# Optimization experiments

Measured on AMD Instinct MI355X. Metric: run time of the kernel, lower is better.

The kernel has to match this reference:

```python
import jax, jax.numpy as jnp
import numpy as np

K = 32            # spatial kernel: neighbors per anchor
STRIDE = 4        # spatial_stride -> S = N // 4 anchors
TK_HALF = 1       # temporal_kernel_size=3 -> window offsets -1,0,+1


def setup_inputs() -> dict:
    key = jax.random.key(0)
    k1, k2, k3 = jax.random.split(key, 3)
    points = jax.random.normal(k1, (2, 4, 8192, 6), dtype=jnp.float32)
    # conv_d: Conv2d(4 -> 64, 1x1, bias=False) as a dense matrix [out,in]
    Wd = jax.random.normal(k2, (64, 4), dtype=jnp.float32) * 0.1
    # mlp: Conv2d(64 -> 128, 1x1, bias=False)
    Wm = jax.random.normal(k3, (128, 64), dtype=jnp.float32) * 0.1
    return {"points": points, "Wd": Wd, "Wm": Wm}


def _fps(xyz, npoint):
    """Farthest point sampling on a single frame. xyz: [N,3] -> idx [npoint] int32.
    Deterministic start at index 0."""
    d0 = jnp.sum((xyz - xyz[0]) ** 2, axis=-1)  # [N]

    def body(dists, _):
        nxt = jnp.argmax(dists)
        d = jnp.sum((xyz - xyz[nxt]) ** 2, axis=-1)
        return jnp.minimum(dists, d), nxt.astype(jnp.int32)

    _, idxs = jax.lax.scan(body, d0, None, length=npoint - 1)
    return jnp.concatenate([jnp.zeros((1,), jnp.int32), idxs])


def _knn_idx(neighbor_xyz, anchor_xyz, k):
    """Adaptive ball query realized as k-nearest-neighbors.
    neighbor_xyz: [B,N,3], anchor_xyz: [B,S,3] -> idx [B,S,k]."""
    d2 = jnp.sum((anchor_xyz[:, :, None, :] - neighbor_xyz[:, None, :, :]) ** 2, axis=-1)  # [B,S,N]
    _, idx = jax.lax.top_k(-d2, k)
    return idx


def _group(pts, idx):
    """pts: [B,N,C], idx: [B,S,K] -> [B,S,K,C] gather per batch."""
    return jax.vmap(lambda p, i: p[i])(pts, idx)


def reference(points, Wd, Wm):
    xyzs = points[..., :3]                       # [B,L,N,3] (rgb unused when in_planes==0)
    B, L, N, _ = xyzs.shape
    S = N // STRIDE
    # replicate temporal padding [1,1]
    pad = jnp.concatenate([xyzs[:, :1], xyzs, xyzs[:, -1:]], axis=1)  # [B,L+2,N,3]

    new_xyzs, new_feats = [], []
    for t in range(TK_HALF, L + 2 - TK_HALF):    # anchor frames in padded indexing
        frame = pad[:, t]                        # [B,N,3]
        aidx = jax.vmap(lambda x: _fps(x, S))(frame)       # [B,S]
        anchor = _group(frame, aidx[:, :, None])[:, :, 0]  # [B,S,3]

        fsum = jnp.zeros((B, S, Wm.shape[0]), dtype=points.dtype)
        for di in range(-TK_HALF, TK_HALF + 1):
            nb = pad[:, t + di]                              # [B,N,3]
            idx = _knn_idx(nb, anchor, K)                    # [B,S,K]
            grouped = _group(nb, idx)                        # [B,S,K,3]
            disp = grouped - anchor[:, :, None, :]           # xyz displacement
            tdisp = jnp.full((B, S, K, 1), float(di), dtype=points.dtype)
            d4 = jnp.concatenate([disp, tdisp], axis=-1)     # [B,S,K,4]
            h = jax.nn.relu(jnp.einsum('bskc,oc->bsko', d4, Wd))   # conv_d + ReLU
            h = jax.nn.relu(jnp.einsum('bsko,po->bskp', h, Wm))    # mlp + ReLU
            fsum = fsum + jnp.max(h, axis=2)                 # spatial max-pool, temporal sum
        new_xyzs.append(anchor)
        new_feats.append(fsum)

    new_xyzs = jnp.stack(new_xyzs, axis=1)                   # [B,T,S,3]
    new_feats = jnp.stack(new_feats, axis=1).transpose(0, 1, 3, 2)  # [B,T,C,S]
    return new_xyzs, new_feats
```

## Files before the change

kernel.cpp:

```cpp
#include <hip/hip_runtime.h>
#include <stdint.h>

#define NPTS 8192
#define NS   2048
#define KNNK 32

typedef unsigned long long u64;

__global__ __launch_bounds__(512)
void fps_kernel(const float* __restrict__ pts,
                float* __restrict__ out_xyz)
{
    const int bt  = blockIdx.x;
    const int tid = threadIdx.x;
    const float* frame = pts + (size_t)bt * NPTS * 6;

    __shared__ float4 p4[NPTS];
    __shared__ u64 ring[3];

    float px[16], py[16], pz[16], d[16];
#pragma unroll
    for (int j = 0; j < 16; ++j) {
        int n = j * 512 + tid;
        float x = frame[n*6+0], y = frame[n*6+1], z = frame[n*6+2];
        px[j] = x; py[j] = y; pz[j] = z;
        d[j]  = 3.4028234663852886e38f;
        p4[n] = make_float4(x, y, z, 0.0f);
    }
    if (tid < 3) ring[tid] = 0;
    if (tid == 0) {
        float* ow = out_xyz + (size_t)bt * NS * 3;
        ow[0] = px[0]; ow[1] = py[0]; ow[2] = pz[0];
    }
    __syncthreads();
    float sx = p4[0].x, sy = p4[0].y, sz = p4[0].z;

    int r = 1;
    for (int i = 1; i < NS; ++i) {
        float mloc = 0.0f;
#pragma unroll
        for (int j = 0; j < 16; ++j) {
            float dx = __fsub_rn(px[j], sx);
            float dy = __fsub_rn(py[j], sy);
            float dz = __fsub_rn(pz[j], sz);
            float d2 = __fadd_rn(__fadd_rn(__fmul_rn(dx,dx), __fmul_rn(dy,dy)),
                                 __fmul_rn(dz,dz));
            float nd = fminf(d[j], d2);
            d[j] = nd;
            mloc = fmaxf(mloc, nd);
        }
        int bestn = 0;
#pragma unroll
        for (int j = 15; j >= 0; --j)
            bestn = (d[j] == mloc) ? (j * 512 + tid) : bestn;
        u64 key = ((u64)__float_as_uint(mloc) << 32) | (unsigned)(8191 - bestn);
#pragma unroll
        for (int off = 32; off > 0; off >>= 1) {
            u64 o = __shfl_xor(key, off, 64);
            key = (o > key) ? o : key;
        }
        if ((tid & 63) == 0) atomicMax(&ring[r], key);
        int rn = r + 1; if (rn == 3) rn = 0;
        if (tid == 0) ring[rn] = 0;
        __syncthreads();
        u64 k = ring[r];
        int idx = 8191 - (int)(k & 0xFFFFFFFFu);
        float4 c = p4[idx];
        sx = c.x; sy = c.y; sz = c.z;
        if (tid == 0) {
            float* ow = out_xyz + ((size_t)bt * NS + i) * 3;
            ow[0] = sx; ow[1] = sy; ow[2] = sz;
        }
        r = rn;
    }
}

__device__ __forceinline__ void knn_compact(u64* st, int lane, int& cnt, u64& rk)
{
    for (int e = 0; e < 32; ++e)
        if (e >= cnt) st[(e + 32) * 64 + lane] = ~0ull;
    for (int k = 2; k <= 32; k <<= 1)
        for (int j = k >> 1; j > 0; j >>= 1)
            for (int i = 0; i < 32; ++i) {
                int l = i ^ j;
                if (l > i) {
                    u64 a = st[(i + 32) * 64 + lane];
                    u64 b = st[(l + 32) * 64 + lane];
                    bool asc = ((i & k) == 0);
                    if ((a > b) == asc) {
                        st[(i + 32) * 64 + lane] = b;
                        st[(l + 32) * 64 + lane] = a;
                    }
                }
            }
    for (int i = 0; i < 32; ++i) {
        u64 a = st[i * 64 + lane];
        u64 b = st[(63 - i) * 64 + lane];
        if (b < a) st[i * 64 + lane] = b;
    }
    for (int j = 16; j > 0; j >>= 1)
        for (int i = 0; i < 32; ++i) {
            int l = i ^ j;
            if (l > i) {
                u64 a = st[i * 64 + lane];
                u64 b = st[l * 64 + lane];
                if (a > b) {
                    st[i * 64 + lane] = b;
                    st[l * 64 + lane] = a;
                }
            }
        }
    rk = st[31 * 64 + lane];
    cnt = 0;
}

__global__ __launch_bounds__(64)
void knn_kernel(const float* __restrict__ pts,
                const float* __restrict__ anchors,
                unsigned short* __restrict__ knn_out)
{
    const int blk  = blockIdx.x;
    const int bt   = blk / 96;
    const int r    = blk % 96;
    const int di   = r / 32;
    const int sblk = r % 32;
    const int b = bt >> 2, t0 = bt & 3;
    int lnb = t0 + di - 1; lnb = lnb < 0 ? 0 : (lnb > 3 ? 3 : lnb);
    const float* nb = pts + (size_t)(b * 4 + lnb) * NPTS * 6;
    const int lane = threadIdx.x;
    const int s    = sblk * 64 + lane;

    const float* ap = anchors + ((size_t)bt * NS + s) * 3;
    float ax = ap[0], ay = ap[1], az = ap[2];

    __shared__ u64 st[65 * 64];
    __shared__ float4 tile[512];

    for (int e = 0; e < 64; ++e) st[e * 64 + lane] = ~0ull;
    u64 rk = ~0ull;
    int cnt = 0;

    for (int tb = 0; tb < NPTS; tb += 512) {
        __syncthreads();
#pragma unroll
        for (int q = 0; q < 8; ++q) {
            int c = q * 64 + lane;
            int n = tb + c;
            tile[c] = make_float4(nb[n*6+0], nb[n*6+1], nb[n*6+2], 0.0f);
        }
        __syncthreads();
        for (int c0 = 0; c0 < 512; c0 += 8) {
#pragma unroll
            for (int j = 0; j < 8; ++j) {
                float4 qv = tile[c0 + j];
                float dx = __fsub_rn(ax, qv.x);
                float dy = __fsub_rn(ay, qv.y);
                float dz = __fsub_rn(az, qv.z);
                float d2 = __fadd_rn(__fadd_rn(__fmul_rn(dx,dx), __fmul_rn(dy,dy)),
                                     __fmul_rn(dz,dz));
                u64 key = ((u64)__float_as_uint(d2) << 32)
                        | (unsigned)(tb + c0 + j);
                bool p = key < rk;
                int row = p ? (32 + cnt) : 64;
                st[row * 64 + lane] = key;
                cnt += p ? 1 : 0;
            }
            if (__any(cnt >= 24)) knn_compact(st, lane, cnt, rk);
        }
    }
    knn_compact(st, lane, cnt, rk);

    unsigned short* op = knn_out + (((size_t)bt * 3 + di) * NS + s) * KNNK;
#pragma unroll
    for (int e = 0; e < 32; ++e)
        op[e] = (unsigned short)(st[e * 64 + lane] & 0xFFFFull);
}

__global__ __launch_bounds__(256)
void mlp_kernel(const float* __restrict__ pts,
                const float* __restrict__ anchors,
                const unsigned short* __restrict__ knn,
                const float* __restrict__ Wd,
                const float* __restrict__ Wm,
                float* __restrict__ out_feats)
{
    const int blk   = blockIdx.x;
    const int bt    = blk >> 10;
    const int spair = blk & 1023;
    const int b = bt >> 2, t0 = bt & 3;
    const int tid = threadIdx.x;
    const int a   = tid >> 7;
    const int p   = tid & 127;
    const int s   = spair * 2 + a;

    __shared__ float WmT[64 * 128];
    __shared__ float Wds[256];
    __shared__ float h1[2][64][36];
    __shared__ float d4s[2][32][4];

    for (int i = tid; i < 8192; i += 256) {
        int pp = i >> 6, oo = i & 63;
        WmT[oo * 128 + pp] = Wm[i];
    }
    Wds[tid & 255] = Wd[tid & 255];

    float fsum = 0.0f;

    for (int dd = 0; dd < 3; ++dd) {
        __syncthreads();
        if (tid < 64) {
            int sa = tid >> 5, k = tid & 31;
            int ss = spair * 2 + sa;
            int lnb = t0 + dd - 1; lnb = lnb < 0 ? 0 : (lnb > 3 ? 3 : lnb);
            const float* nbf = pts + (size_t)(b*4 + lnb) * NPTS * 6;
            const float* ap = anchors + ((size_t)bt * NS + ss) * 3;
            int idx = knn[(((size_t)bt*3 + dd) * NS + ss) * KNNK + k];
            d4s[sa][k][0] = nbf[idx*6+0] - ap[0];
            d4s[sa][k][1] = nbf[idx*6+1] - ap[1];
            d4s[sa][k][2] = nbf[idx*6+2] - ap[2];
            d4s[sa][k][3] = (float)(dd - 1);
        }
        __syncthreads();
        {
            int k  = tid & 31;
            int oq = (tid >> 5) & 3;
            float4 dv = *(const float4*)&d4s[a][k][0];
#pragma unroll
            for (int ii = 0; ii < 16; ++ii) {
                int o = oq * 16 + ii;
                float4 w = *(const float4*)&Wds[o * 4];
                float h = fmaf(dv.x, w.x, fmaf(dv.y, w.y, fmaf(dv.z, w.z, dv.w * w.w)));
                h1[a][o][k] = fmaxf(h, 0.0f);
            }
        }
        __syncthreads();
        float acc[32];
#pragma unroll
        for (int kk = 0; kk < 32; ++kk) acc[kk] = 0.0f;
        for (int o = 0; o < 64; ++o) {
            float wmv = WmT[o * 128 + p];
            const float4* hp = (const float4*)&h1[a][o][0];
#pragma unroll
            for (int kk = 0; kk < 8; ++kk) {
                float4 hv = hp[kk];
                acc[kk*4+0] = fmaf(wmv, hv.x, acc[kk*4+0]);
                acc[kk*4+1] = fmaf(wmv, hv.y, acc[kk*4+1]);
                acc[kk*4+2] = fmaf(wmv, hv.z, acc[kk*4+2]);
                acc[kk*4+3] = fmaf(wmv, hv.w, acc[kk*4+3]);
            }
        }
        float mx = acc[0];
#pragma unroll
        for (int kk = 1; kk < 32; ++kk) mx = fmaxf(mx, acc[kk]);
        fsum += fmaxf(mx, 0.0f);
    }
    out_feats[((size_t)bt * 128 + p) * NS + s] = fsum;
}

extern "C" void kernel_launch(void* const* d_in, const int* in_sizes, int n_in,
                              void* d_out, int out_size, void* d_ws, size_t ws_size,
                              hipStream_t stream)
{
    const float* pts = (const float*)d_in[0];
    const float* Wd  = (const float*)d_in[1];
    const float* Wm  = (const float*)d_in[2];

    float* out_xyz   = (float*)d_out;
    float* out_feats = out_xyz + 8 * NS * 3;

    unsigned short* knn = (unsigned short*)d_ws;

    fps_kernel<<<8, 512, 0, stream>>>(pts, out_xyz);
    knn_kernel<<<8 * 3 * 32, 64, 0, stream>>>(pts, out_xyz, knn);
    mlp_kernel<<<8 * (NS / 2), 256, 0, stream>>>(pts, out_xyz, knn, Wd, Wm, out_feats);
}
```

Baseline: 3.498 ms.

## Vectorize FPS with packed floats, split KNN across two waves, register-tile MLP

Result: slower. 3.603 ms (+3.0%).

```diff
diff --git a/kernel.cpp b/kernel.cpp
--- a/kernel.cpp
+++ b/kernel.cpp
@@ -6,11 +6,13 @@
 #define KNNK 32
 
 typedef unsigned long long u64;
+typedef float f32x2 __attribute__((ext_vector_type(2)));
 
 __global__ __launch_bounds__(512)
 void fps_kernel(const float* __restrict__ pts,
                 float* __restrict__ out_xyz)
 {
+#pragma clang fp contract(off)
     const int bt  = blockIdx.x;
     const int tid = threadIdx.x;
     const float* frame = pts + (size_t)bt * NPTS * 6;
@@ -18,41 +20,47 @@
     __shared__ float4 p4[NPTS];
     __shared__ u64 ring[3];
 
-    float px[16], py[16], pz[16], d[16];
+    f32x2 x2[8], y2[8], z2[8], dd2[8];
 #pragma unroll
     for (int j = 0; j < 16; ++j) {
         int n = j * 512 + tid;
         float x = frame[n*6+0], y = frame[n*6+1], z = frame[n*6+2];
-        px[j] = x; py[j] = y; pz[j] = z;
-        d[j]  = 3.4028234663852886e38f;
+        x2[j >> 1][j & 1] = x;
+        y2[j >> 1][j & 1] = y;
+        z2[j >> 1][j & 1] = z;
+        dd2[j >> 1][j & 1] = 3.4028234663852886e38f;
         p4[n] = make_float4(x, y, z, 0.0f);
     }
     if (tid < 3) ring[tid] = 0;
     if (tid == 0) {
         float* ow = out_xyz + (size_t)bt * NS * 3;
-        ow[0] = px[0]; ow[1] = py[0]; ow[2] = pz[0];
+        ow[0] = x2[0][0]; ow[1] = y2[0][0]; ow[2] = z2[0][0];
     }
     __syncthreads();
     float sx = p4[0].x, sy = p4[0].y, sz = p4[0].z;
 
     int r = 1;
     for (int i = 1; i < NS; ++i) {
-        float mloc = 0.0f;
-#pragma unroll
-        for (int j = 0; j < 16; ++j) {
-            float dx = __fsub_rn(px[j], sx);
-            float dy = __fsub_rn(py[j], sy);
-            float dz = __fsub_rn(pz[j], sz);
-            float d2 = __fadd_rn(__fadd_rn(__fmul_rn(dx,dx), __fmul_rn(dy,dy)),
-                                 __fmul_rn(dz,dz));
-            float nd = fminf(d[j], d2);
-            d[j] = nd;
-            mloc = fmaxf(mloc, nd);
-        }
+        f32x2 sxv = {sx, sx}, syv = {sy, sy}, szv = {sz, sz};
+        f32x2 m2 = {0.0f, 0.0f};
+#pragma unroll
+        for (int q = 0; q < 8; ++q) {
+            f32x2 dx = x2[q] - sxv;
+            f32x2 dy = y2[q] - syv;
+            f32x2 dz = z2[q] - szv;
+            f32x2 dd = (dx*dx + dy*dy) + dz*dz;
+            f32x2 nd;
+            nd[0] = fminf(dd2[q][0], dd[0]);
+            nd[1] = fminf(dd2[q][1], dd[1]);
+            dd2[q] = nd;
+            m2[0] = fmaxf(m2[0], nd[0]);
+            m2[1] = fmaxf(m2[1], nd[1]);
+        }
+        float mloc = fmaxf(m2[0], m2[1]);
         int bestn = 0;
 #pragma unroll
         for (int j = 15; j >= 0; --j)
-            bestn = (d[j] == mloc) ? (j * 512 + tid) : bestn;
+            bestn = (dd2[j >> 1][j & 1] == mloc) ? (j * 512 + tid) : bestn;
         u64 key = ((u64)__float_as_uint(mloc) << 32) | (unsigned)(8191 - bestn);
 #pragma unroll
         for (int off = 32; off > 0; off >>= 1) {
@@ -75,7 +83,7 @@
     }
 }
 
-__device__ __forceinline__ void knn_compact(u64* st, int lane, int& cnt, u64& rk)
+__device__ __forceinline__ void knn_compact(u64* st, int lane, int& cnt, float& rk_f)
 {
     for (int e = 0; e < 32; ++e)
         if (e >= cnt) st[(e + 32) * 64 + lane] = ~0ull;
@@ -110,70 +118,82 @@
                 }
             }
         }
-    rk = st[31 * 64 + lane];
+    rk_f = __uint_as_float((unsigned)(st[31 * 64 + lane] >> 32));
     cnt = 0;
 }
 
-__global__ __launch_bounds__(64)
+__global__ __launch_bounds__(128)
 void knn_kernel(const float* __restrict__ pts,
                 const float* __restrict__ anchors,
                 unsigned short* __restrict__ knn_out)
 {
     const int blk  = blockIdx.x;
     const int bt   = blk / 96;
-    const int r    = blk % 96;
-    const int di   = r / 32;
-    const int sblk = r % 32;
+    const int rr   = blk % 96;
+    const int di   = rr / 32;
+    const int sblk = rr % 32;
     const int b = bt >> 2, t0 = bt & 3;
     int lnb = t0 + di - 1; lnb = lnb < 0 ? 0 : (lnb > 3 ? 3 : lnb);
     const float* nb = pts + (size_t)(b * 4 + lnb) * NPTS * 6;
-    const int lane = threadIdx.x;
+    const int tid  = threadIdx.x;
+    const int w    = tid >> 6;
+    const int lane = tid & 63;
     const int s    = sblk * 64 + lane;
 
     const float* ap = anchors + ((size_t)bt * NS + s) * 3;
     float ax = ap[0], ay = ap[1], az = ap[2];
 
-    __shared__ u64 st[65 * 64];
-    __shared__ float4 tile[512];
-
-    for (int e = 0; e < 64; ++e) st[e * 64 + lane] = ~0ull;
-    u64 rk = ~0ull;
+    __shared__ u64 st[2][64 * 64];
+    __shared__ u64 trash[64];
+    __shared__ float4 tile[2][256];
+    u64* stw = st[w];
+
+    for (int e = 0; e < 64; ++e) stw[e * 64 + lane] = ~0ull;
+    float rk_f = __uint_as_float(0xFFFFFFFFu);
     int cnt = 0;
 
-    for (int tb = 0; tb < NPTS; tb += 512) {
-        __syncthreads();
-#pragma unroll
-        for (int q = 0; q < 8; ++q) {
+    const int cbase = w * 4096;
+    for (int tb = 0; tb < 16; ++tb) {
+        __syncthreads();
+#pragma unroll
+        for (int q = 0; q < 4; ++q) {
             int c = q * 64 + lane;
-            int n = tb + c;
-            tile[c] = make_float4(nb[n*6+0], nb[n*6+1], nb[n*6+2], 0.0f);
-        }
-        __syncthreads();
-        for (int c0 = 0; c0 < 512; c0 += 8) {
+            int n = cbase + tb * 256 + c;
+            tile[w][c] = make_float4(nb[n*6+0], nb[n*6+1], nb[n*6+2], 0.0f);
+        }
+        __syncthreads();
+        for (int c0 = 0; c0 < 256; c0 += 8) {
 #pragma unroll
             for (int j = 0; j < 8; ++j) {
-                float4 qv = tile[c0 + j];
+                float4 qv = tile[w][c0 + j];
                 float dx = __fsub_rn(ax, qv.x);
                 float dy = __fsub_rn(ay, qv.y);
                 float dz = __fsub_rn(az, qv.z);
                 float d2 = __fadd_rn(__fadd_rn(__fmul_rn(dx,dx), __fmul_rn(dy,dy)),
                                      __fmul_rn(dz,dz));
                 u64 key = ((u64)__float_as_uint(d2) << 32)
-                        | (unsigned)(tb + c0 + j);
-                bool p = key < rk;
-                int row = p ? (32 + cnt) : 64;
-                st[row * 64 + lane] = key;
+                        | (unsigned)(cbase + tb * 256 + c0 + j);
+                bool p = !(d2 > rk_f);
+                u64* dst = p ? &stw[(32 + cnt) * 64 + lane] : &trash[lane];
+                *dst = key;
                 cnt += p ? 1 : 0;
             }
-            if (__any(cnt >= 24)) knn_compact(st, lane, cnt, rk);
-        }
-    }
-    knn_compact(st, lane, cnt, rk);
-
-    unsigned short* op = knn_out + (((size_t)bt * 3 + di) * NS + s) * KNNK;
-#pragma unroll
-    for (int e = 0; e < 32; ++e)
-        op[e] = (unsigned short)(st[e * 64 + lane] & 0xFFFFull);
+            if (__any(cnt >= 24)) knn_compact(stw, lane, cnt, rk_f);
+        }
+    }
+    knn_compact(stw, lane, cnt, rk_f);
+    __syncthreads();
+
+    if (w == 0) {
+        unsigned short* op = knn_out + (((size_t)bt * 3 + di) * NS + s) * KNNK;
+#pragma unroll
+        for (int e = 0; e < 32; ++e) {
+            u64 a = st[0][e * 64 + lane];
+            u64 c = st[1][(31 - e) * 64 + lane];
+            u64 m = c < a ? c : a;
+            op[e] = (unsigned short)(m & 0xFFFFull);
+        }
+    }
 }
 
 __global__ __launch_bounds__(256)
@@ -184,33 +204,37 @@
                 const float* __restrict__ Wm,
                 float* __restrict__ out_feats)
 {
-    const int blk   = blockIdx.x;
-    const int bt    = blk >> 10;
-    const int spair = blk & 1023;
+    const int blk = blockIdx.x;
+    const int bt  = blk >> 9;
+    const int sq  = blk & 511;
     const int b = bt >> 2, t0 = bt & 3;
     const int tid = threadIdx.x;
-    const int a   = tid >> 7;
-    const int p   = tid & 127;
-    const int s   = spair * 2 + a;
+    const int a   = tid >> 6;
+    const int r   = tid & 63;
+    const int p0  = (r & 15) * 8;
+    const int kt  = r >> 4;
+    const int k0  = kt * 8;
+    const int s   = sq * 4 + a;
 
     __shared__ float WmT[64 * 128];
     __shared__ float Wds[256];
-    __shared__ float h1[2][64][36];
-    __shared__ float d4s[2][32][4];
+    __shared__ float h1[4][64][32];
+    __shared__ float d4s[4][32][4];
+    __shared__ float pmax[4][4][128];
 
     for (int i = tid; i < 8192; i += 256) {
         int pp = i >> 6, oo = i & 63;
         WmT[oo * 128 + pp] = Wm[i];
     }
-    Wds[tid & 255] = Wd[tid & 255];
-
-    float fsum = 0.0f;
+    Wds[tid] = Wd[tid];
+
+    float fsum0 = 0.0f, fsum1 = 0.0f;
 
     for (int dd = 0; dd < 3; ++dd) {
         __syncthreads();
-        if (tid < 64) {
+        if (tid < 128) {
             int sa = tid >> 5, k = tid & 31;
-            int ss = spair * 2 + sa;
+            int ss = sq * 4 + sa;
             int lnb = t0 + dd - 1; lnb = lnb < 0 ? 0 : (lnb > 3 ? 3 : lnb);
             const float* nbf = pts + (size_t)(b*4 + lnb) * NPTS * 6;
             const float* ap = anchors + ((size_t)bt * NS + ss) * 3;
@@ -222,39 +246,62 @@
         }
         __syncthreads();
         {
-            int k  = tid & 31;
-            int oq = (tid >> 5) & 3;
+            int k  = r & 31;
+            int oh = r >> 5;
             float4 dv = *(const float4*)&d4s[a][k][0];
 #pragma unroll
-            for (int ii = 0; ii < 16; ++ii) {
-                int o = oq * 16 + ii;
-                float4 w = *(const float4*)&Wds[o * 4];
-                float h = fmaf(dv.x, w.x, fmaf(dv.y, w.y, fmaf(dv.z, w.z, dv.w * w.w)));
+            for (int ii = 0; ii < 32; ++ii) {
+                int o = oh * 32 + ii;
+                float4 wv = *(const float4*)&Wds[o * 4];
+                float h = fmaf(dv.x, wv.x, fmaf(dv.y, wv.y,
+                             fmaf(dv.z, wv.z, dv.w * wv.w)));
                 h1[a][o][k] = fmaxf(h, 0.0f);
             }
         }
         __syncthreads();
-        float acc[32];
-#pragma unroll
-        for (int kk = 0; kk < 32; ++kk) acc[kk] = 0.0f;
+        float acc[8][8];
+#pragma unroll
+        for (int i = 0; i < 8; ++i)
+#pragma unroll
+            for (int j = 0; j < 8; ++j) acc[i][j] = 0.0f;
         for (int o = 0; o < 64; ++o) {
-            float wmv = WmT[o * 128 + p];
-            const float4* hp = (const float4*)&h1[a][o][0];
-#pragma unroll
-            for (int kk = 0; kk < 8; ++kk) {
-                float4 hv = hp[kk];
-                acc[kk*4+0] = fmaf(wmv, hv.x, acc[kk*4+0]);
-                acc[kk*4+1] = fmaf(wmv, hv.y, acc[kk*4+1]);
-                acc[kk*4+2] = fmaf(wmv, hv.z, acc[kk*4+2]);
-                acc[kk*4+3] = fmaf(wmv, hv.w, acc[kk*4+3]);
-            }
-        }
-        float mx = acc[0];
-#pragma unroll
-        for (int kk = 1; kk < 32; ++kk) mx = fmaxf(mx, acc[kk]);
-        fsum += fmaxf(mx, 0.0f);
-    }
-    out_feats[((size_t)bt * 128 + p) * NS + s] = fsum;
+            float4 wv0 = *(const float4*)&WmT[o * 128 + p0];
+            float4 wv1 = *(const float4*)&WmT[o * 128 + p0 + 4];
+            float4 h0 = *(const float4*)&h1[a][o][k0];
+            float4 h4 = *(const float4*)&h1[a][o][k0 + 4];
+            float hw[8] = {h0.x, h0.y, h0.z, h0.w, h4.x, h4.y, h4.z, h4.w};
+#pragma unroll
+            for (int i = 0; i < 8; ++i) {
+                float ww = (i < 4) ? ((i == 0) ? wv0.x : (i == 1) ? wv0.y :
+                                      (i == 2) ? wv0.z : wv0.w)
+                                   : ((i == 4) ? wv1.x : (i == 5) ? wv1.y :
+                                      (i == 6) ? wv1.z : wv1.w);
+#pragma unroll
+                for (int j = 0; j < 8; ++j)
+                    acc[i][j] = fmaf(ww, hw[j], acc[i][j]);
+            }
+        }
+        float4 pmA, pmB;
+#pragma unroll
+        for (int i = 0; i < 8; ++i) {
+            float m = acc[i][0];
+#pragma unroll
+            for (int j = 1; j < 8; ++j) m = fmaxf(m, acc[i][j]);
+            if (i < 4) ((float*)&pmA)[i] = m;
+            else       ((float*)&pmB)[i - 4] = m;
+        }
+        *(float4*)&pmax[a][kt][p0]     = pmA;
+        *(float4*)&pmax[a][kt][p0 + 4] = pmB;
+        __syncthreads();
+        float m0 = fmaxf(fmaxf(pmax[a][0][r], pmax[a][1][r]),
+                         fmaxf(pmax[a][2][r], pmax[a][3][r]));
+        float m1 = fmaxf(fmaxf(pmax[a][0][r + 64], pmax[a][1][r + 64]),
+                         fmaxf(pmax[a][2][r + 64], pmax[a][3][r + 64]));
+        fsum0 += fmaxf(m0, 0.0f);
+        fsum1 += fmaxf(m1, 0.0f);
+    }
+    out_feats[((size_t)bt * 128 + r) * NS + s]        = fsum0;
+    out_feats[((size_t)bt * 128 + r + 64) * NS + s]   = fsum1;
 }
 
 extern "C" void kernel_launch(void* const* d_in, const int* in_sizes, int n_in,
@@ -271,6 +318,6 @@
     unsigned short* knn = (unsigned short*)d_ws;
 
     fps_kernel<<<8, 512, 0, stream>>>(pts, out_xyz);
-    knn_kernel<<<8 * 3 * 32, 64, 0, stream>>>(pts, out_xyz, knn);
-    mlp_kernel<<<8 * (NS / 2), 256, 0, stream>>>(pts, out_xyz, knn, Wd, Wm, out_feats);
-}
+    knn_kernel<<<8 * 3 * 32, 128, 0, stream>>>(pts, out_xyz, knn);
+    mlp_kernel<<<8 * (NS / 4), 256, 0, stream>>>(pts, out_xyz, knn, Wd, Wm, out_feats);
+}
```
